# Kernel optimization log

Measured on AMD Instinct MI355X. Metric: run time of the kernel, lower is better.

The kernel has to match this reference:

```python
import jax, jax.numpy as jnp
import numpy as np

D_MODEL = 768
D_STATE = 16
D_CONV = 4
EXPAND = 2
N_LAYERS = 2
HEADDIM = 64
PATCH_DIM = 256
D_INNER = EXPAND * D_MODEL            # 1536
NHEADS = D_INNER // HEADDIM           # 24
CONV_DIM = D_INNER + 2 * D_STATE      # 1568 (x, B, C share the conv)
D_IN_PROJ = 2 * D_INNER + 2 * D_STATE + NHEADS  # 3128


def _mamba2(u, w_in, conv_w, conv_b, dt_bias, A_log, D, norm_w, w_out):
    """Mamba2 block (ngroups=1, rmsnorm=True, non-fused reference path)."""
    b, l, _ = u.shape
    zxbcdt = u @ w_in                                   # (b,l,D_IN_PROJ)
    z = zxbcdt[..., :D_INNER]
    xBC = zxbcdt[..., D_INNER:D_INNER + CONV_DIM]
    dt = jax.nn.softplus(zxbcdt[..., D_INNER + CONV_DIM:] + dt_bias)  # (b,l,H)
    # causal depthwise conv1d over L, then silu
    kernel = conv_w.T[:, None, :]                       # (D_CONV,1,CONV_DIM)
    xBC = jax.lax.conv_general_dilated(
        xBC, kernel, (1,), [(D_CONV - 1, 0)],
        dimension_numbers=('NLC', 'LIO', 'NLC'),
        feature_group_count=CONV_DIM) + conv_b
    xBC = jax.nn.silu(xBC)
    x = xBC[..., :D_INNER].reshape(b, l, NHEADS, HEADDIM)
    B = xBC[..., D_INNER:D_INNER + D_STATE]             # (b,l,N)
    C = xBC[..., D_INNER + D_STATE:]                    # (b,l,N)
    A = -jnp.exp(A_log)                                 # (H,)

    def step(h, inp):
        dt_t, x_t, b_t, c_t = inp                       # (b,H),(b,H,P),(b,N),(b,N)
        dA = jnp.exp(dt_t * A)                          # (b,H)
        h = h * dA[:, :, None, None] + jnp.einsum('bh,bhp,bn->bhpn', dt_t, x_t, b_t)
        y_t = jnp.einsum('bhpn,bn->bhp', h, c_t)
        return h, y_t

    h0 = jnp.zeros((b, NHEADS, HEADDIM, D_STATE), u.dtype)
    _, y = jax.lax.scan(step, h0,
                        (dt.swapaxes(0, 1), x.swapaxes(0, 1),
                         B.swapaxes(0, 1), C.swapaxes(0, 1)))
    y = y.swapaxes(0, 1) + x * D[:, None]               # skip: D per head
    y = y.reshape(b, l, D_INNER)
    # gated RMSNorm: rmsnorm(y * silu(z)) * weight
    g = y * jax.nn.silu(z)
    g = g * jax.lax.rsqrt(jnp.mean(g * g, axis=-1, keepdims=True) + 1e-5)
    y = g * norm_w
    return y @ w_out


def _backbone(patch_embeddings, Wp, bp, in_w, conv_w, conv_b, dt_bias,
              A_log, Dh, norm_w, out_w, bi_w, ls, fin_w):
    x = patch_embeddings @ Wp + bp
    for i in range(N_LAYERS):
        h_f = _mamba2(x, in_w[i, 0], conv_w[i, 0], conv_b[i, 0], dt_bias[i, 0],
                      A_log[i, 0], Dh[i, 0], norm_w[i, 0], out_w[i, 0])
        h_b = jnp.flip(_mamba2(jnp.flip(x, 1), in_w[i, 1], conv_w[i, 1],
                               conv_b[i, 1], dt_bias[i, 1], A_log[i, 1],
                               Dh[i, 1], norm_w[i, 1], out_w[i, 1]), 1)
        m = jnp.concatenate([h_f, h_b], axis=-1) @ bi_w[i]
        x = x + m * ls[i]
    # final RMSNorm with unit offset
    v = jnp.mean(x * x, axis=-1, keepdims=True)
    return x * jax.lax.rsqrt(v + 1e-6) * (1.0 + fin_w)


def setup_inputs() -> dict:
    key = jax.random.key(0)
    ks = jax.random.split(key, 14)
    L2 = (N_LAYERS, 2)
    pe = jax.random.normal(ks[0], (2, 2048, PATCH_DIM), jnp.float32)
    Wp = jax.random.normal(ks[1], (PATCH_DIM, D_MODEL), jnp.float32) * 0.02
    bp = jnp.zeros((D_MODEL,), jnp.float32)
    in_w = jax.random.normal(ks[2], L2 + (D_MODEL, D_IN_PROJ), jnp.float32) * 0.02
    conv_w = jax.random.normal(ks[3], L2 + (CONV_DIM, D_CONV), jnp.float32) * 0.2
    conv_b = jnp.zeros(L2 + (CONV_DIM,), jnp.float32)
    dt_bias = jax.random.uniform(ks[4], L2 + (NHEADS,), jnp.float32, -4.0, -2.0)
    A_log = jnp.log(jax.random.uniform(ks[5], L2 + (NHEADS,), jnp.float32, 1.0, 16.0))
    Dh = jax.random.normal(ks[6], L2 + (NHEADS,), jnp.float32) * 0.1 + 1.0
    norm_w = jnp.ones(L2 + (D_INNER,), jnp.float32)
    out_w = jax.random.normal(ks[7], L2 + (D_INNER, D_MODEL), jnp.float32) * 0.02
    bi_w = jax.random.normal(ks[8], (N_LAYERS, 2 * D_MODEL, D_MODEL), jnp.float32) * 0.02
    ls = jnp.full((N_LAYERS, D_MODEL), 1e-4, jnp.float32)
    fin_w = jnp.zeros((D_MODEL,), jnp.float32)
    return {"patch_embeddings": pe, "Wp": Wp, "bp": bp, "in_w": in_w,
            "conv_w": conv_w, "conv_b": conv_b, "dt_bias": dt_bias,
            "A_log": A_log, "Dh": Dh, "norm_w": norm_w, "out_w": out_w,
            "bi_w": bi_w, "ls": ls, "fin_w": fin_w}


def reference(patch_embeddings, Wp, bp, in_w, conv_w, conv_b, dt_bias,
              A_log, Dh, norm_w, out_w, bi_w, ls, fin_w):
    return _backbone(patch_embeddings, Wp, bp, in_w, conv_w, conv_b, dt_bias,
                     A_log, Dh, norm_w, out_w, bi_w, ls, fin_w)
```

## Files before the change

kernel.cpp:

```cpp
#include <hip/hip_runtime.h>

typedef unsigned short u16;
typedef short s16x8 __attribute__((ext_vector_type(8)));
typedef u16 u16x8 __attribute__((ext_vector_type(8)));
typedef float f32x4 __attribute__((ext_vector_type(4)));

__device__ inline float bf2f(u16 u) {
    union { unsigned int i; float f; } w; w.i = ((unsigned int)u) << 16; return w.f;
}
__device__ inline u16 f2bf(float f) {
    union { float f; unsigned int i; } w; w.f = f;
    unsigned int u = w.i;
    u += 0x7fffu + ((u >> 16) & 1u);
    return (u16)(u >> 16);
}

__global__ __launch_bounds__(256)
void wtransT(const float* __restrict__ src, u16* __restrict__ dst,
             int K, int N, int dstride, int src_z, int dz_hi, int dz_lo)
{
    int z = blockIdx.z;
    src += (size_t)z * src_z;
    dst += (size_t)(z >> 1) * dz_hi + (size_t)(z & 1) * dz_lo;
    __shared__ float t[32][33];
    int kt = blockIdx.y * 32, nt0 = blockIdx.x * 32;
    int lx = threadIdx.x & 31, ly = threadIdx.x >> 5;
#pragma unroll
    for (int i = 0; i < 32; i += 8) {
        int k = kt + ly + i, n = nt0 + lx;
        t[ly + i][lx] = (k < K && n < N) ? src[(size_t)k * N + n] : 0.f;
    }
    __syncthreads();
#pragma unroll
    for (int i = 0; i < 32; i += 8) {
        int n = nt0 + ly + i, k = kt + lx;
        if (n < N && k < K) dst[(size_t)n * dstride + k] = f2bf(t[lx][ly + i]);
    }
}

__global__ void cvtk(const float* __restrict__ src, u16* __restrict__ dst, int n) {
    int i = blockIdx.x * 256 + threadIdx.x;
    if (i < n) dst[i] = f2bf(src[i]);
}

__global__ __launch_bounds__(256, 2)
void gemm8(const u16* __restrict__ A, const u16* __restrict__ WT,
           int M, int N, int K,
           u16* __restrict__ bout, int ostride)
{
    __shared__ u16 lds8[2 * 16384];

    int mt, nt;
    {
        int nwg = gridDim.x * gridDim.y;
        int f = blockIdx.y * gridDim.x + blockIdx.x;
        int q = nwg >> 3, r = nwg & 7;
        int xcd = f & 7, lo = f >> 3;
        int wid = (xcd < r ? xcd * (q + 1) : r * (q + 1) + (xcd - r) * q) + lo;
        mt = wid % gridDim.y; nt = wid / gridDim.y;
    }

    const int tid  = threadIdx.x;
    const int lane = tid & 63;
    const int wave = tid >> 6;
    const int wm = wave >> 1, wn = wave & 1;
    const int r16 = lane & 15;
    const int lg  = lane >> 4;
    const int mb  = mt * 128;
    const int nb  = nt * 128;
    const int wbase = tid & 192;

    f32x4 acc[4][4];
#pragma unroll
    for (int mi = 0; mi < 4; mi++)
#pragma unroll
        for (int ni = 0; ni < 4; ni++)
            acc[mi][ni] = (f32x4){0.f, 0.f, 0.f, 0.f};

    auto stage = [&](int buf, int k0) {
        u16* bA = &lds8[buf * 16384];
        u16* bB = bA + 8192;
#pragma unroll
        for (int r = 0; r < 4; r++) {
            int e = r * 256 + tid;
            int row = e >> 3;
            int cbs = (e & 7) ^ (row & 7);
            const u16* g = A + (size_t)(mb + row) * K + k0 + cbs * 8;
            __builtin_amdgcn_global_load_lds(
                (const __attribute__((address_space(1))) void*)g,
                (__attribute__((address_space(3))) void*)&bA[(r * 256 + wbase) * 8],
                16, 0, 0);
        }
#pragma unroll
        for (int r = 0; r < 4; r++) {
            int e = r * 256 + tid;
            int row = e >> 3;
            int cbs = (e & 7) ^ (row & 7);
            const u16* g = WT + (size_t)(nb + row) * K + k0 + cbs * 8;
            __builtin_amdgcn_global_load_lds(
                (const __attribute__((address_space(1))) void*)g,
                (__attribute__((address_space(3))) void*)&bB[(r * 256 + wbase) * 8],
                16, 0, 0);
        }
    };

    const int ntk = K >> 6;
    stage(0, 0);
    stage(1, 64);
    asm volatile("s_waitcnt vmcnt(8)" ::: "memory");
    __builtin_amdgcn_sched_barrier(0);
    __builtin_amdgcn_s_barrier();

    for (int t = 0; t < ntk; t++) {
        const int buf = t & 1;
        const u16* bA = &lds8[buf * 16384];
        const u16* bB = bA + 8192;
        s16x8 a[4][2], b[4][2];
#pragma unroll
        for (int mf = 0; mf < 4; mf++)
#pragma unroll
            for (int kk = 0; kk < 2; kk++) {
                int row = wm * 64 + mf * 16 + r16;
                int cb = (kk * 4 + lg) ^ (row & 7);
                a[mf][kk] = *(const s16x8*)&bA[row * 64 + cb * 8];
            }
#pragma unroll
        for (int nf = 0; nf < 4; nf++)
#pragma unroll
            for (int kk = 0; kk < 2; kk++) {
                int row = wn * 64 + nf * 16 + r16;
                int cb = (kk * 4 + lg) ^ (row & 7);
                b[nf][kk] = *(const s16x8*)&bB[row * 64 + cb * 8];
            }
        asm volatile("s_waitcnt lgkmcnt(0)" ::: "memory");
        __builtin_amdgcn_sched_barrier(0);
        __builtin_amdgcn_s_barrier();
        if (t + 2 < ntk) {
            stage(buf, (t + 2) << 6);
            asm volatile("s_waitcnt vmcnt(8)" ::: "memory");
        } else {
            asm volatile("s_waitcnt vmcnt(0)" ::: "memory");
        }
        __builtin_amdgcn_sched_barrier(0);
        __builtin_amdgcn_s_barrier();
        __builtin_amdgcn_s_setprio(1);
#pragma unroll
        for (int mf = 0; mf < 4; mf++)
#pragma unroll
            for (int nf = 0; nf < 4; nf++) {
                acc[mf][nf] = __builtin_amdgcn_mfma_f32_16x16x32_bf16(
                    a[mf][0], b[nf][0], acc[mf][nf], 0, 0, 0);
                acc[mf][nf] = __builtin_amdgcn_mfma_f32_16x16x32_bf16(
                    a[mf][1], b[nf][1], acc[mf][nf], 0, 0, 0);
            }
        __builtin_amdgcn_s_setprio(0);
    }

#pragma unroll
    for (int mf = 0; mf < 4; mf++) {
        const int rowb = mb + wm * 64 + mf * 16 + lg * 4;
#pragma unroll
        for (int nf = 0; nf < 4; nf++) {
            int col = nb + wn * 64 + nf * 16 + r16;
            if (col < N) {
#pragma unroll
                for (int j = 0; j < 4; j++)
                    bout[(size_t)(rowb + j) * ostride + col] = f2bf(acc[mf][nf][j]);
            }
        }
    }
}

__global__ __launch_bounds__(256, 2)
void gemm9(const u16* __restrict__ A, const u16* __restrict__ WT, int K,
           float* __restrict__ fout, u16* __restrict__ bout,
           const float* __restrict__ lsv)
{
    __shared__ u16 lds9[2 * 12288];

    int mt, nt;
    {
        int nwg = gridDim.x * gridDim.y;
        int f = blockIdx.y * gridDim.x + blockIdx.x;
        int q = nwg >> 3, r = nwg & 7;
        int xcd = f & 7, lo = f >> 3;
        int wid = (xcd < r ? xcd * (q + 1) : r * (q + 1) + (xcd - r) * q) + lo;
        mt = wid % gridDim.y; nt = wid / gridDim.y;
    }

    const int tid  = threadIdx.x;
    const int lane = tid & 63;
    const int wave = tid >> 6;
    const int wm = wave >> 1, wn = wave & 1;
    const int r16 = lane & 15;
    const int lg  = lane >> 4;
    const int mb  = mt * 128;
    const int nb  = nt * 64;
    const int wbase = tid & 192;

    f32x4 acc[4][2];
#pragma unroll
    for (int mi = 0; mi < 4; mi++)
#pragma unroll
        for (int ni = 0; ni < 2; ni++)
            acc[mi][ni] = (f32x4){0.f, 0.f, 0.f, 0.f};

    auto stage = [&](int buf, int k0) {
        u16* bA = &lds9[buf * 12288];
#pragma unroll
        for (int rr = 0; rr < 6; rr++) {
            int e = rr * 256 + tid;
            int row = e >> 3;
            int cbs = (e & 7) ^ (row & 7);
            const u16* g = (rr < 4)
                ? A  + (size_t)(mb + row) * K + k0 + cbs * 8
                : WT + (size_t)(nb + row - 128) * K + k0 + cbs * 8;
            __builtin_amdgcn_global_load_lds(
                (const __attribute__((address_space(1))) void*)g,
                (__attribute__((address_space(3))) void*)&bA[(rr * 256 + wbase) * 8],
                16, 0, 0);
        }
    };

    const int ntk = K >> 6;
    stage(0, 0);
    stage(1, 64);
    asm volatile("s_waitcnt vmcnt(6)" ::: "memory");
    __builtin_amdgcn_sched_barrier(0);
    __builtin_amdgcn_s_barrier();

    for (int t = 0; t < ntk; t++) {
        const int buf = t & 1;
        const u16* bA = &lds9[buf * 12288];
        const u16* bB = bA + 8192;
        s16x8 a[4][2], b[2][2];
#pragma unroll
        for (int mf = 0; mf < 4; mf++)
#pragma unroll
            for (int kk = 0; kk < 2; kk++) {
                int row = wm * 64 + mf * 16 + r16;
                int cb = (kk * 4 + lg) ^ (row & 7);
                a[mf][kk] = *(const s16x8*)&bA[row * 64 + cb * 8];
            }
#pragma unroll
        for (int nf = 0; nf < 2; nf++)
#pragma unroll
            for (int kk = 0; kk < 2; kk++) {
                int row = wn * 32 + nf * 16 + r16;
                int cb = (kk * 4 + lg) ^ (row & 7);
                b[nf][kk] = *(const s16x8*)&bB[row * 64 + cb * 8];
            }
        asm volatile("s_waitcnt lgkmcnt(0)" ::: "memory");
        __builtin_amdgcn_sched_barrier(0);
        __builtin_amdgcn_s_barrier();
        if (t + 2 < ntk) {
            stage(buf, (t + 2) << 6);
            asm volatile("s_waitcnt vmcnt(6)" ::: "memory");
        } else {
            asm volatile("s_waitcnt vmcnt(0)" ::: "memory");
        }
        __builtin_amdgcn_sched_barrier(0);
        __builtin_amdgcn_s_barrier();
        __builtin_amdgcn_s_setprio(1);
#pragma unroll
        for (int mf = 0; mf < 4; mf++)
#pragma unroll
            for (int nf = 0; nf < 2; nf++) {
                acc[mf][nf] = __builtin_amdgcn_mfma_f32_16x16x32_bf16(
                    a[mf][0], b[nf][0], acc[mf][nf], 0, 0, 0);
                acc[mf][nf] = __builtin_amdgcn_mfma_f32_16x16x32_bf16(
                    a[mf][1], b[nf][1], acc[mf][nf], 0, 0, 0);
            }
        __builtin_amdgcn_s_setprio(0);
    }

#pragma unroll
    for (int mf = 0; mf < 4; mf++) {
        const int rowb = mb + wm * 64 + mf * 16 + lg * 4;
#pragma unroll
        for (int nf = 0; nf < 2; nf++) {
            int col = nb + wn * 32 + nf * 16 + r16;
#pragma unroll
            for (int j = 0; j < 4; j++) {
                size_t o = (size_t)(rowb + j) * 768 + col;
                float xv = fout[o] + acc[mf][nf][j] * lsv[col];
                fout[o] = xv; bout[o] = f2bf(xv);
            }
        }
    }
}

template<int BM, int BN, int EPI>
__global__ __launch_bounds__(256)
void gemmL(const u16* __restrict__ A, const u16* __restrict__ WT,
           int M, int N, int K,
           float* __restrict__ fout, u16* __restrict__ bout,
           const float* __restrict__ bias, const float* __restrict__ lsv,
           int ostride, int ocoloff,
           size_t aZ, size_t wZ, size_t oZ, int ocolZ)
{
    constexpr int MI = BM / 32, NI = BN / 32;
    constexpr int BUF = (BM + BN) * 32;
    constexpr int RA = BM / 64, RB = BN / 64;
    __shared__ u16 lds[2 * BUF];

    {
        int z = blockIdx.z;
        A += (size_t)z * aZ; WT += (size_t)z * wZ;
        bout += (size_t)(z >> 1) * oZ; ocoloff += (z & 1) * ocolZ;
    }

    int mt, nt;
    {
        int nwg = gridDim.x * gridDim.y;
        int f = blockIdx.y * gridDim.x + blockIdx.x;
        int q = nwg >> 3, r = nwg & 7;
        int xcd = f & 7, lo = f >> 3;
        int wid = (xcd < r ? xcd * (q + 1) : r * (q + 1) + (xcd - r) * q) + lo;
        mt = wid % gridDim.y; nt = wid / gridDim.y;
    }

    const int tid  = threadIdx.x;
    const int lane = tid & 63;
    const int wave = tid >> 6;
    const int wm = wave >> 1, wn = wave & 1;
    const int r16 = lane & 15;
    const int ks  = (lane >> 4) * 8;
    const int mb  = mt * BM;
    const int nb  = nt * BN;
    const int wbase = tid & 192;

    f32x4 acc[MI][NI];
#pragma unroll
    for (int mi = 0; mi < MI; mi++)
#pragma unroll
        for (int ni = 0; ni < NI; ni++)
            acc[mi][ni] = (f32x4){0.f, 0.f, 0.f, 0.f};

    auto stage = [&](int buf, int k0) {
        u16* bufA = &lds[buf * BUF];
        u16* bufB = &lds[buf * BUF + BM * 32];
#pragma unroll
        for (int r = 0; r < RA; r++) {
            int c = r * 256 + tid;
            const u16* g = A + (size_t)(mb + (c >> 2)) * K + k0 + (c & 3) * 8;
            __builtin_amdgcn_global_load_lds(
                (const __attribute__((address_space(1))) void*)g,
                (__attribute__((address_space(3))) void*)&bufA[(r * 256 + wbase) * 8],
                16, 0, 0);
        }
#pragma unroll
        for (int r = 0; r < RB; r++) {
            int c = r * 256 + tid;
            const u16* g = WT + (size_t)(nb + (c >> 2)) * K + k0 + (c & 3) * 8;
            __builtin_amdgcn_global_load_lds(
                (const __attribute__((address_space(1))) void*)g,
                (__attribute__((address_space(3))) void*)&bufB[(r * 256 + wbase) * 8],
                16, 0, 0);
        }
    };
    auto compute = [&](int buf) {
        const u16* bufA = &lds[buf * BUF];
        const u16* bufB = &lds[buf * BUF + BM * 32];
        s16x8 af[MI], bfr[NI];
#pragma unroll
        for (int mi = 0; mi < MI; mi++)
            af[mi] = *(const s16x8*)&bufA[(wm * (BM / 2) + mi * 16 + r16) * 32 + ks];
#pragma unroll
        for (int ni = 0; ni < NI; ni++)
            bfr[ni] = *(const s16x8*)&bufB[(wn * (BN / 2) + ni * 16 + r16) * 32 + ks];
#pragma unroll
        for (int mi = 0; mi < MI; mi++)
#pragma unroll
            for (int ni = 0; ni < NI; ni++)
                acc[mi][ni] = __builtin_amdgcn_mfma_f32_16x16x32_bf16(
                    af[mi], bfr[ni], acc[mi][ni], 0, 0, 0);
    };

    const int nt2 = K >> 5;
    stage(0, 0);
    __syncthreads();
    for (int t = 0; t < nt2; t++) {
        if (t + 1 < nt2) stage((t + 1) & 1, (t + 1) << 5);
        compute(t & 1);
        __syncthreads();
    }

#pragma unroll
    for (int mi = 0; mi < MI; mi++) {
        const int rowb = mb + wm * (BM / 2) + mi * 16 + (lane >> 4) * 4;
#pragma unroll
        for (int ni = 0; ni < NI; ni++) {
            int col = nb + wn * (BN / 2) + ni * 16 + r16;
            if (col < N) {
#pragma unroll
                for (int j = 0; j < 4; j++) {
                    int row = rowb + j;
                    float v = acc[mi][ni][j];
                    if (EPI == 0) {
                        v += bias[col];
                        size_t o = (size_t)row * ostride + col;
                        fout[o] = v; bout[o] = f2bf(v);
                    } else if (EPI == 1) {
                        bout[(size_t)row * ostride + ocoloff + col] = f2bf(v);
                    } else {
                        size_t o = (size_t)row * 768 + col;
                        float xv = fout[o] + v * lsv[col];
                        fout[o] = xv; bout[o] = f2bf(xv);
                    }
                }
            }
        }
    }
}

__global__ void dtk(const u16* __restrict__ zxAll, float* __restrict__ dtAll,
                    const float* __restrict__ dtb)
{
    int idx = blockIdx.x * 256 + threadIdx.x;
    if (idx >= 2 * 4096 * 24) return;
    int dir = idx / (4096 * 24);
    int r   = idx % (4096 * 24);
    int row = r / 24, h = r % 24;
    float raw = bf2f(zxAll[(size_t)row * 6256 + dir * 3128 + 3104 + h]) + dtb[dir * 24 + h];
    dtAll[((size_t)dir * 4096 + row) * 24 + h] = raw > 20.f ? raw : log1pf(__expf(raw));
}

__global__ __launch_bounds__(256)
void scan1k(const u16* __restrict__ zxAll, const float* __restrict__ dtAll,
            const float* __restrict__ cw, const float* __restrict__ cb,
            const float* __restrict__ Alog, const float* __restrict__ Dhp,
            u16* __restrict__ yAll, float* __restrict__ states, float* __restrict__ decays)
{
    const int c   = blockIdx.x;
    const int bh  = blockIdx.y;
    const int dir = blockIdx.z;
    const int b = bh / 24, h = bh % 24;
    const float* dtp = dtAll + (size_t)dir * 4096 * 24;
    u16* yp = yAll + dir * 1536;
    const float Av = -__expf(Alog[dir * 24 + h]);
    const float Dv = Dhp[dir * 24 + h];
    const int inst = (dir * 2 + b) * 24 + h;

    const int tid  = threadIdx.x;
    const int lane = tid & 63;
    const int wave = tid >> 6;
    const int r16  = lane & 15;
    const int ks   = (lane >> 4) * 8;

    __shared__ u16 xT[64][72];
    __shared__ u16 Gs[64][72];
    __shared__ u16 Bs[64][40];
    __shared__ u16 Cs[64][40];
    __shared__ u16 SBT[16][72];
    __shared__ float dts[64], cds[64];

    const u16* zxd = zxAll + dir * 3128 + 1536;
    auto growp = [&](int ii) -> const u16* {
        int l = dir ? (2047 - ii) : ii;
        return zxd + ((size_t)b * 2048 + l) * 6256;
    };
    auto rowof = [&](int t) -> size_t {
        int i = c * 64 + t;
        int l = dir ? (2047 - i) : i;
        return (size_t)b * 2048 + l;
    };
    const u16x8 zz = {0,0,0,0,0,0,0,0};

    {
        int tr = tid >> 2, pg = tid & 3;
        int chb = h * 64 + pg * 16;
        int i0 = c * 64 + tr;
        u16x8 tv[4][2];
#pragma unroll
        for (int k = 0; k < 4; k++) {
            int ii = i0 - 3 + k;
            if (ii >= 0) {
                const u16* s = growp(ii) + chb;
                tv[k][0] = *(const u16x8*)s;
                tv[k][1] = *(const u16x8*)(s + 8);
            } else { tv[k][0] = zz; tv[k][1] = zz; }
        }
        const float* cwp = cw + ((size_t)dir * 1568 + chb) * 4;
        const float* cbp = cb + (size_t)dir * 1568 + chb;
#pragma unroll
        for (int j = 0; j < 16; j++) {
            f32x4 wj = *(const f32x4*)(cwp + j * 4);
            float a = cbp[j];
            int hi = j >> 3, lo2 = j & 7;
            a += bf2f(tv[0][hi][lo2]) * wj[0] + bf2f(tv[1][hi][lo2]) * wj[1]
               + bf2f(tv[2][hi][lo2]) * wj[2] + bf2f(tv[3][hi][lo2]) * wj[3];
            a = a / (1.f + __expf(-a));
            xT[pg * 16 + j][tr] = f2bf(a);
        }
    }
    {
        int t = tid & 63, which = tid >> 6;
        if (which < 2) {
            int chb = 1536 + which * 16;
            int i0 = c * 64 + t;
            u16x8 tv[4][2];
#pragma unroll
            for (int k = 0; k < 4; k++) {
                int ii = i0 - 3 + k;
                if (ii >= 0) {
                    const u16* s = growp(ii) + chb;
                    tv[k][0] = *(const u16x8*)s;
                    tv[k][1] = *(const u16x8*)(s + 8);
                } else { tv[k][0] = zz; tv[k][1] = zz; }
            }
            const float* cwp = cw + ((size_t)dir * 1568 + chb) * 4;
            const float* cbp = cb + (size_t)dir * 1568 + chb;
            u16* dst = which ? &Cs[t][0] : &Bs[t][0];
#pragma unroll
            for (int j = 0; j < 16; j++) {
                f32x4 wj = *(const f32x4*)(cwp + j * 4);
                float a = cbp[j];
                int hi = j >> 3, lo2 = j & 7;
                a += bf2f(tv[0][hi][lo2]) * wj[0] + bf2f(tv[1][hi][lo2]) * wj[1]
                   + bf2f(tv[2][hi][lo2]) * wj[2] + bf2f(tv[3][hi][lo2]) * wj[3];
                a = a / (1.f + __expf(-a));
                dst[j] = f2bf(a);
            }
        } else {
            u16* dst = (which == 2) ? &Bs[t][16] : &Cs[t][16];
            *(u16x8*)dst = zz; *(u16x8*)(dst + 8) = zz;
        }
    }
    if (tid < 64) {
        float v = dtp[rowof(tid) * 24 + h];
        dts[tid] = v;
        float s = v;
#pragma unroll
        for (int o = 1; o < 64; o <<= 1) {
            float nvl = __shfl_up(s, o, 64);
            if (lane >= o) s += nvl;
        }
        cds[tid] = s;
    }
    __syncthreads();

    {
        const s16x8 af = *(const s16x8*)&Cs[wave * 16 + r16][ks];
#pragma unroll
        for (int st = 0; st < 4; st++) {
            const s16x8 bfr = *(const s16x8*)&Bs[st * 16 + r16][ks];
            f32x4 a2 = {0.f, 0.f, 0.f, 0.f};
            a2 = __builtin_amdgcn_mfma_f32_16x16x32_bf16(af, bfr, a2, 0, 0, 0);
            int s = st * 16 + (lane & 15);
            int tbase = wave * 16 + (lane >> 4) * 4;
            float cs = cds[s], dtv = dts[s];
#pragma unroll
            for (int j = 0; j < 4; j++) {
                int t = tbase + j;
                float g = 0.f;
                if (s <= t) {
                    g = a2[j] * dtv * __expf(Av * (cds[t] - cs));
                    if (s == t) g += Dv;
                }
                Gs[t][s] = f2bf(g);
            }
        }
    }
    {
        float cdT = cds[63];
        int s = tid & 63;
        float sc = __expf(Av * (cdT - cds[s])) * dts[s];
#pragma unroll
        for (int it = 0; it < 4; it++) {
            int n = (tid >> 6) + it * 4;
            SBT[n][s] = f2bf(sc * bf2f(Bs[s][n]));
        }
    }
    __syncthreads();

    {
#pragma unroll
        for (int pt = 0; pt < 4; pt++) {
            f32x4 a2 = {0.f, 0.f, 0.f, 0.f};
#pragma unroll
            for (int kk = 0; kk < 2; kk++) {
                s16x8 af = *(const s16x8*)&Gs[wave * 16 + r16][kk * 32 + ks];
                s16x8 bfr = *(const s16x8*)&xT[pt * 16 + r16][kk * 32 + ks];
                a2 = __builtin_amdgcn_mfma_f32_16x16x32_bf16(af, bfr, a2, 0, 0, 0);
            }
            int p = pt * 16 + (lane & 15);
            int tbase = wave * 16 + (lane >> 4) * 4;
#pragma unroll
            for (int j = 0; j < 4; j++) {
                size_t row = rowof(tbase + j);
                yp[row * 3072 + h * 64 + p] = f2bf(a2[j]);
            }
        }
    }
    {
        f32x4 a2 = {0.f, 0.f, 0.f, 0.f};
#pragma unroll
        for (int kk = 0; kk < 2; kk++) {
            s16x8 af = *(const s16x8*)&xT[wave * 16 + r16][kk * 32 + ks];
            s16x8 bfr = *(const s16x8*)&SBT[r16][kk * 32 + ks];
            a2 = __builtin_amdgcn_mfma_f32_16x16x32_bf16(af, bfr, a2, 0, 0, 0);
        }
        int n = lane & 15;
        int pbase = wave * 16 + (lane >> 4) * 4;
        float* st = states + ((size_t)inst * 32 + c) * 1024;
#pragma unroll
        for (int j = 0; j < 4; j++) st[(pbase + j) * 16 + n] = a2[j];
        if (tid == 0) decays[inst * 32 + c] = __expf(Av * cds[63]);
    }
}

__global__ __launch_bounds__(256)
void scan2k(float* __restrict__ states, const float* __restrict__ decays)
{
    int inst = blockIdx.x;
    int tid = threadIdx.x;
    float* base = states + (size_t)inst * 32 * 1024 + tid * 4;
    const float* dec = decays + inst * 32;
    f32x4 hreg = {0.f, 0.f, 0.f, 0.f};
    f32x4 L = *(f32x4*)base;
    for (int cc = 0; cc < 32; cc++) {
        f32x4 Lnext;
        if (cc + 1 < 32) Lnext = *(f32x4*)(base + (cc + 1) * 1024);
        *(f32x4*)(base + cc * 1024) = hreg;
        float d = dec[cc];
        hreg = hreg * d + L;
        L = Lnext;
    }
}

__global__ __launch_bounds__(256)
void scan3k(const float* __restrict__ states,
            const u16* __restrict__ zxAll, const float* __restrict__ dtAll,
            const float* __restrict__ cw, const float* __restrict__ cb,
            const float* __restrict__ Alog, u16* __restrict__ yAll)
{
    const int c   = blockIdx.x + 1;
    const int bh  = blockIdx.y;
    const int dir = blockIdx.z;
    const int b = bh / 24, h = bh % 24;
    const float* dtp = dtAll + (size_t)dir * 4096 * 24;
    u16* yp = yAll + dir * 1536;
    const float Av = -__expf(Alog[dir * 24 + h]);
    const int inst = (dir * 2 + b) * 24 + h;
    const int tid = threadIdx.x;

    __shared__ float hs[64][20];
    __shared__ u16 Cs3[64][16];
    __shared__ float ets[64];

    const u16* zxd = zxAll + dir * 3128 + 1536;
    auto growp = [&](int ii) -> const u16* {
        int l = dir ? (2047 - ii) : ii;
        return zxd + ((size_t)b * 2048 + l) * 6256;
    };
    auto rowof = [&](int t) -> size_t {
        int i = c * 64 + t;
        int l = dir ? (2047 - i) : i;
        return (size_t)b * 2048 + l;
    };

    {
        const float* sp = states + ((size_t)inst * 32 + c) * 1024 + tid * 4;
        f32x4 v = *(const f32x4*)sp;
        int e = tid * 4;
        int p = e >> 4, n = e & 15;
        hs[p][n] = v[0]; hs[p][n+1] = v[1]; hs[p][n+2] = v[2]; hs[p][n+3] = v[3];
    }
    if (tid < 64) {
        int i0 = c * 64 + tid;
        u16x8 tv[4][2];
#pragma unroll
        for (int k = 0; k < 4; k++) {
            const u16* s = growp(i0 - 3 + k) + 1552;
            tv[k][0] = *(const u16x8*)s;
            tv[k][1] = *(const u16x8*)(s + 8);
        }
        const float* cwp = cw + ((size_t)dir * 1568 + 1552) * 4;
        const float* cbp = cb + (size_t)dir * 1568 + 1552;
#pragma unroll
        for (int j = 0; j < 16; j++) {
            f32x4 wj = *(const f32x4*)(cwp + j * 4);
            float a = cbp[j];
            int hi = j >> 3, lo2 = j & 7;
            a += bf2f(tv[0][hi][lo2]) * wj[0] + bf2f(tv[1][hi][lo2]) * wj[1]
               + bf2f(tv[2][hi][lo2]) * wj[2] + bf2f(tv[3][hi][lo2]) * wj[3];
            a = a / (1.f + __expf(-a));
            Cs3[tid][j] = f2bf(a);
        }
        float v = dtp[rowof(tid) * 24 + h];
        float s = v;
#pragma unroll
        for (int o = 1; o < 64; o <<= 1) {
            float nvl = __shfl_up(s, o, 64);
            if ((tid & 63) >= o) s += nvl;
        }
        ets[tid] = __expf(Av * s);
    }
    __syncthreads();

    int t = tid >> 2, pg = tid & 3;
    float cv[16];
    float et = ets[t];
#pragma unroll
    for (int n = 0; n < 16; n++) cv[n] = bf2f(Cs3[t][n]) * et;
    size_t row = rowof(t);
    u16* yrow = yp + row * 3072 + h * 64 + pg * 16;
    u16x8 ya = *(u16x8*)yrow;
    u16x8 yb = *(u16x8*)(yrow + 8);
#pragma unroll
    for (int jj = 0; jj < 16; jj++) {
        int p = pg * 16 + jj;
        float acc = 0.f;
#pragma unroll
        for (int q = 0; q < 4; q++) {
            f32x4 hv = *(const f32x4*)&hs[p][q * 4];
            acc += cv[q*4]*hv[0] + cv[q*4+1]*hv[1] + cv[q*4+2]*hv[2] + cv[q*4+3]*hv[3];
        }
        if (jj < 8) ya[jj] = f2bf(bf2f(ya[jj]) + acc);
        else        yb[jj - 8] = f2bf(bf2f(yb[jj - 8]) + acc);
    }
    *(u16x8*)yrow = ya;
    *(u16x8*)(yrow + 8) = yb;
}

__global__ __launch_bounds__(256)
void gatek(const u16* __restrict__ zxAll, u16* __restrict__ yAll,
           const float* __restrict__ nw)
{
    int row = blockIdx.x, dir = blockIdx.y;
    const u16* zx = zxAll + (size_t)row * 6256 + dir * 3128;
    u16* y = yAll + (size_t)row * 3072 + dir * 1536;
    const float* nwp = nw + dir * 1536;
    int tid = threadIdx.x;
    float g[6]; float s = 0.f;
#pragma unroll
    for (int j = 0; j < 6; j++) {
        int c = j * 256 + tid;
        float z  = bf2f(zx[c]);
        float yv = bf2f(y[c]);
        float gv = yv * z / (1.f + __expf(-z));
        g[j] = gv; s += gv * gv;
    }
    __shared__ float red[4];
    for (int o = 32; o; o >>= 1) s += __shfl_down(s, o, 64);
    if ((tid & 63) == 0) red[tid >> 6] = s;
    __syncthreads();
    s = red[0] + red[1] + red[2] + red[3];
    float sc = rsqrtf(s * (1.f / 1536.f) + 1e-5f);
#pragma unroll
    for (int j = 0; j < 6; j++) {
        int c = j * 256 + tid;
        y[c] = f2bf(g[j] * sc * nwp[c]);
    }
}

__global__ __launch_bounds__(256)
void finalk(const float* __restrict__ x, const float* __restrict__ fw, float* __restrict__ out)
{
    int row = blockIdx.x; int tid = threadIdx.x;
    const float* xr = x + (size_t)row * 768;
    float v[3]; float s = 0.f;
#pragma unroll
    for (int j = 0; j < 3; j++) {
        int c = j * 256 + tid;
        v[j] = xr[c]; s += v[j] * v[j];
    }
    __shared__ float red[4];
    for (int o = 32; o; o >>= 1) s += __shfl_down(s, o, 64);
    if ((tid & 63) == 0) red[tid >> 6] = s;
    __syncthreads();
    s = red[0] + red[1] + red[2] + red[3];
    float sc = rsqrtf(s * (1.f / 768.f) + 1e-6f);
#pragma unroll
    for (int j = 0; j < 3; j++) {
        int c = j * 256 + tid;
        out[(size_t)row * 768 + c] = v[j] * sc * (1.f + fw[c]);
    }
}

extern "C" void kernel_launch(void* const* d_in, const int* in_sizes, int n_in,
                              void* d_out, int out_size, void* d_ws, size_t ws_size,
                              hipStream_t stream)
{
    const float* pe      = (const float*)d_in[0];
    const float* Wp      = (const float*)d_in[1];
    const float* bp      = (const float*)d_in[2];
    const float* in_w    = (const float*)d_in[3];
    const float* conv_w  = (const float*)d_in[4];
    const float* conv_b  = (const float*)d_in[5];
    const float* dt_bias = (const float*)d_in[6];
    const float* A_log   = (const float*)d_in[7];
    const float* Dh      = (const float*)d_in[8];
    const float* norm_w  = (const float*)d_in[9];
    const float* out_w   = (const float*)d_in[10];
    const float* bi_w    = (const float*)d_in[11];
    const float* ls      = (const float*)d_in[12];
    const float* fin_w   = (const float*)d_in[13];

    char* wp = (char*)d_ws;
    auto alloc = [&](size_t bytes) {
        char* r = wp; wp += (bytes + 255) & ~(size_t)255; return r;
    };
    u16*   WpT    = (u16*)  alloc((size_t)768 * 256 * 2);
    u16*   inWT   = (u16*)  alloc((size_t)2 * 6272 * 768 * 2);
    u16*   outWB  = (u16*)  alloc((size_t)4 * 1536 * 768 * 2);
    u16*   biWT   = (u16*)  alloc((size_t)4 * 768 * 768 * 2);
    u16*   WcombT = (u16*)  alloc((size_t)2 * 768 * 3072 * 2);
    u16*   peB    = (u16*)  alloc((size_t)4096 * 256 * 2);
    float* x      = (float*)alloc((size_t)4096 * 768 * 4);
    u16*   xb     = (u16*)  alloc((size_t)4096 * 768 * 2);
    u16*   zxAll  = (u16*)  alloc((size_t)4096 * 6256 * 2);
    float* dtAll  = (float*)alloc((size_t)2 * 4096 * 24 * 4);
    u16*   yAll   = (u16*)  alloc((size_t)4096 * 3072 * 2);
    float* states = (float*)alloc((size_t)96 * 32 * 1024 * 4);
    float* decays = (float*)alloc((size_t)96 * 32 * 4);

    wtransT<<<dim3(24, 8, 1), 256, 0, stream>>>(Wp, WpT, 256, 768, 256, 0, 0, 0);
    wtransT<<<dim3(98, 24, 4), 256, 0, stream>>>(in_w, inWT, 768, 3128, 768,
                                                 2402304, 4816896, 2402304);
    wtransT<<<dim3(24, 24, 4), 256, 0, stream>>>(bi_w, biWT, 768, 768, 768,
                                                 589824, 1179648, 589824);
    cvtk<<<(4 * 1536 * 768 + 255) / 256, 256, 0, stream>>>(out_w, outWB, 4 * 1536 * 768);
    cvtk<<<4096, 256, 0, stream>>>(pe, peB, 4096 * 256);

    gemmL<64, 64, 1><<<dim3(24, 12, 4), 256, 0, stream>>>(
        biWT, outWB, 768, 1536, 768, nullptr, WcombT,
        nullptr, nullptr, 3072, 0,
        (size_t)589824, (size_t)1179648, (size_t)768 * 3072, 1536);

    gemmL<64, 64, 0><<<dim3(12, 64, 1), 256, 0, stream>>>(
        peB, WpT, 4096, 768, 256, x, xb, bp, nullptr, 768, 0, 0, 0, 0, 0);

    for (int i = 0; i < 2; i++) {
        gemm8<<<dim3(49, 32, 1), 256, 0, stream>>>(
            xb, inWT + (size_t)i * 6272 * 768, 4096, 6256, 768, zxAll, 6256);
        dtk<<<(2 * 4096 * 24 + 255) / 256, 256, 0, stream>>>(zxAll, dtAll, dt_bias + i * 48);
        scan1k<<<dim3(32, 48, 2), 256, 0, stream>>>(zxAll, dtAll,
                                                    conv_w + (size_t)i * 2 * 1568 * 4,
                                                    conv_b + (size_t)i * 2 * 1568,
                                                    A_log + i * 48, Dh + i * 48,
                                                    yAll, states, decays);
        scan2k<<<96, 256, 0, stream>>>(states, decays);
        scan3k<<<dim3(31, 48, 2), 256, 0, stream>>>(states, zxAll, dtAll,
                                                    conv_w + (size_t)i * 2 * 1568 * 4,
                                                    conv_b + (size_t)i * 2 * 1568,
                                                    A_log + i * 48, yAll);
        gatek<<<dim3(4096, 2), 256, 0, stream>>>(zxAll, yAll, norm_w + (size_t)i * 2 * 1536);
        gemm9<<<dim3(12, 32, 1), 256, 0, stream>>>(
            yAll, WcombT + (size_t)i * 768 * 3072, 3072, x, xb, ls + i * 768);
    }

    finalk<<<4096, 256, 0, stream>>>(x, fin_w, (float*)d_out);
}
```

Baseline: 498.3 us.

## Precompute B/C conv once in preK and specialise small GEMMs with swizzled LDS

```diff
diff --git a/kernel.cpp b/kernel.cpp
--- a/kernel.cpp
+++ b/kernel.cpp
@@ -290,26 +290,18 @@
     }
 }
 
-template<int BM, int BN, int EPI>
-__global__ __launch_bounds__(256)
-void gemmL(const u16* __restrict__ A, const u16* __restrict__ WT,
-           int M, int N, int K,
-           float* __restrict__ fout, u16* __restrict__ bout,
-           const float* __restrict__ bias, const float* __restrict__ lsv,
-           int ostride, int ocoloff,
-           size_t aZ, size_t wZ, size_t oZ, int ocolZ)
-{
-    constexpr int MI = BM / 32, NI = BN / 32;
-    constexpr int BUF = (BM + BN) * 32;
-    constexpr int RA = BM / 64, RB = BN / 64;
-    __shared__ u16 lds[2 * BUF];
+__global__ __launch_bounds__(256, 2)
+void gemm10(const u16* __restrict__ A, const u16* __restrict__ WT, int K,
+            u16* __restrict__ bout, int ostride,
+            size_t aZ, size_t wZ, size_t oZ, int ocolZ)
+{
+    __shared__ u16 ldsA[2 * 12288];
 
     {
         int z = blockIdx.z;
         A += (size_t)z * aZ; WT += (size_t)z * wZ;
-        bout += (size_t)(z >> 1) * oZ; ocoloff += (z & 1) * ocolZ;
-    }
-
+        bout += (size_t)(z >> 1) * oZ + (size_t)(z & 1) * ocolZ;
+    }
     int mt, nt;
     {
         int nwg = gridDim.x * gridDim.y;
@@ -325,109 +317,254 @@
     const int wave = tid >> 6;
     const int wm = wave >> 1, wn = wave & 1;
     const int r16 = lane & 15;
-    const int ks  = (lane >> 4) * 8;
-    const int mb  = mt * BM;
-    const int nb  = nt * BN;
+    const int lg  = lane >> 4;
+    const int mb  = mt * 128;
+    const int nb  = nt * 64;
     const int wbase = tid & 192;
 
-    f32x4 acc[MI][NI];
-#pragma unroll
-    for (int mi = 0; mi < MI; mi++)
-#pragma unroll
-        for (int ni = 0; ni < NI; ni++)
+    f32x4 acc[4][2];
+#pragma unroll
+    for (int mi = 0; mi < 4; mi++)
+#pragma unroll
+        for (int ni = 0; ni < 2; ni++)
             acc[mi][ni] = (f32x4){0.f, 0.f, 0.f, 0.f};
 
     auto stage = [&](int buf, int k0) {
-        u16* bufA = &lds[buf * BUF];
-        u16* bufB = &lds[buf * BUF + BM * 32];
-#pragma unroll
-        for (int r = 0; r < RA; r++) {
-            int c = r * 256 + tid;
-            const u16* g = A + (size_t)(mb + (c >> 2)) * K + k0 + (c & 3) * 8;
+        u16* bA = &ldsA[buf * 12288];
+#pragma unroll
+        for (int rr = 0; rr < 6; rr++) {
+            int e = rr * 256 + tid;
+            int row = e >> 3;
+            int cbs = (e & 7) ^ (row & 7);
+            const u16* g = (rr < 4)
+                ? A  + (size_t)(mb + row) * K + k0 + cbs * 8
+                : WT + (size_t)(nb + row - 128) * K + k0 + cbs * 8;
             __builtin_amdgcn_global_load_lds(
                 (const __attribute__((address_space(1))) void*)g,
-                (__attribute__((address_space(3))) void*)&bufA[(r * 256 + wbase) * 8],
+                (__attribute__((address_space(3))) void*)&bA[(rr * 256 + wbase) * 8],
                 16, 0, 0);
         }
-#pragma unroll
-        for (int r = 0; r < RB; r++) {
-            int c = r * 256 + tid;
-            const u16* g = WT + (size_t)(nb + (c >> 2)) * K + k0 + (c & 3) * 8;
+    };
+
+    const int ntk = K >> 6;
+    stage(0, 0);
+    stage(1, 64);
+    asm volatile("s_waitcnt vmcnt(6)" ::: "memory");
+    __builtin_amdgcn_sched_barrier(0);
+    __builtin_amdgcn_s_barrier();
+
+    for (int t = 0; t < ntk; t++) {
+        const int buf = t & 1;
+        const u16* bA = &ldsA[buf * 12288];
+        const u16* bB = bA + 8192;
+        s16x8 a[4][2], b[2][2];
+#pragma unroll
+        for (int mf = 0; mf < 4; mf++)
+#pragma unroll
+            for (int kk = 0; kk < 2; kk++) {
+                int row = wm * 64 + mf * 16 + r16;
+                int cb = (kk * 4 + lg) ^ (row & 7);
+                a[mf][kk] = *(const s16x8*)&bA[row * 64 + cb * 8];
+            }
+#pragma unroll
+        for (int nf = 0; nf < 2; nf++)
+#pragma unroll
+            for (int kk = 0; kk < 2; kk++) {
+                int row = wn * 32 + nf * 16 + r16;
+                int cb = (kk * 4 + lg) ^ (row & 7);
+                b[nf][kk] = *(const s16x8*)&bB[row * 64 + cb * 8];
+            }
+        asm volatile("s_waitcnt lgkmcnt(0)" ::: "memory");
+        __builtin_amdgcn_sched_barrier(0);
+        __builtin_amdgcn_s_barrier();
+        if (t + 2 < ntk) {
+            stage(buf, (t + 2) << 6);
+            asm volatile("s_waitcnt vmcnt(6)" ::: "memory");
+        } else {
+            asm volatile("s_waitcnt vmcnt(0)" ::: "memory");
+        }
+        __builtin_amdgcn_sched_barrier(0);
+        __builtin_amdgcn_s_barrier();
+        __builtin_amdgcn_s_setprio(1);
+#pragma unroll
+        for (int mf = 0; mf < 4; mf++)
+#pragma unroll
+            for (int nf = 0; nf < 2; nf++) {
+                acc[mf][nf] = __builtin_amdgcn_mfma_f32_16x16x32_bf16(
+                    a[mf][0], b[nf][0], acc[mf][nf], 0, 0, 0);
+                acc[mf][nf] = __builtin_amdgcn_mfma_f32_16x16x32_bf16(
+                    a[mf][1], b[nf][1], acc[mf][nf], 0, 0, 0);
+            }
+        __builtin_amdgcn_s_setprio(0);
+    }
+
+#pragma unroll
+    for (int mf = 0; mf < 4; mf++) {
+        const int rowb = mb + wm * 64 + mf * 16 + lg * 4;
+#pragma unroll
+        for (int nf = 0; nf < 2; nf++) {
+            int col = nb + wn * 32 + nf * 16 + r16;
+#pragma unroll
+            for (int j = 0; j < 4; j++)
+                bout[(size_t)(rowb + j) * ostride + col] = f2bf(acc[mf][nf][j]);
+        }
+    }
+}
+
+__global__ __launch_bounds__(256, 2)
+void gemm11(const u16* __restrict__ A, const u16* __restrict__ WT, int K,
+            float* __restrict__ fout, u16* __restrict__ bout,
+            const float* __restrict__ bias)
+{
+    __shared__ u16 ldsB[2 * 12288];
+
+    int mt, nt;
+    {
+        int nwg = gridDim.x * gridDim.y;
+        int f = blockIdx.y * gridDim.x + blockIdx.x;
+        int q = nwg >> 3, r = nwg & 7;
+        int xcd = f & 7, lo = f >> 3;
+        int wid = (xcd < r ? xcd * (q + 1) : r * (q + 1) + (xcd - r) * q) + lo;
+        mt = wid % gridDim.y; nt = wid / gridDim.y;
+    }
+
+    const int tid  = threadIdx.x;
+    const int lane = tid & 63;
+    const int wave = tid >> 6;
+    const int wm = wave >> 1, wn = wave & 1;
+    const int r16 = lane & 15;
+    const int lg  = lane >> 4;
+    const int mb  = mt * 128;
+    const int nb  = nt * 64;
+    const int wbase = tid & 192;
+
+    f32x4 acc[4][2];
+#pragma unroll
+    for (int mi = 0; mi < 4; mi++)
+#pragma unroll
+        for (int ni = 0; ni < 2; ni++)
+            acc[mi][ni] = (f32x4){0.f, 0.f, 0.f, 0.f};
+
+    auto stage = [&](int buf, int k0) {
+        u16* bA = &ldsB[buf * 12288];
+#pragma unroll
+        for (int rr = 0; rr < 6; rr++) {
+            int e = rr * 256 + tid;
+            int row = e >> 3;
+            int cbs = (e & 7) ^ (row & 7);
+            const u16* g = (rr < 4)
+                ? A  + (size_t)(mb + row) * K + k0 + cbs * 8
+                : WT + (size_t)(nb + row - 128) * K + k0 + cbs * 8;
             __builtin_amdgcn_global_load_lds(
                 (const __attribute__((address_space(1))) void*)g,
-                (__attribute__((address_space(3))) void*)&bufB[(r * 256 + wbase) * 8],
+                (__attribute__((address_space(3))) void*)&bA[(rr * 256 + wbase) * 8],
                 16, 0, 0);
         }
     };
-    auto compute = [&](int buf) {
-        const u16* bufA = &lds[buf * BUF];
-        const u16* bufB = &lds[buf * BUF + BM * 32];
-        s16x8 af[MI], bfr[NI];
-#pragma unroll
-        for (int mi = 0; mi < MI; mi++)
-            af[mi] = *(const s16x8*)&bufA[(wm * (BM / 2) + mi * 16 + r16) * 32 + ks];
-#pragma unroll
-        for (int ni = 0; ni < NI; ni++)
-            bfr[ni] = *(const s16x8*)&bufB[(wn * (BN / 2) + ni * 16 + r16) * 32 + ks];
-#pragma unroll
-        for (int mi = 0; mi < MI; mi++)
-#pragma unroll
-            for (int ni = 0; ni < NI; ni++)
-                acc[mi][ni] = __builtin_amdgcn_mfma_f32_16x16x32_bf16(
-                    af[mi], bfr[ni], acc[mi][ni], 0, 0, 0);
-    };
-
-    const int nt2 = K >> 5;
+
+    const int ntk = K >> 6;
     stage(0, 0);
-    __syncthreads();
-    for (int t = 0; t < nt2; t++) {
-        if (t + 1 < nt2) stage((t + 1) & 1, (t + 1) << 5);
-        compute(t & 1);
-        __syncthreads();
-    }
-
-#pragma unroll
-    for (int mi = 0; mi < MI; mi++) {
-        const int rowb = mb + wm * (BM / 2) + mi * 16 + (lane >> 4) * 4;
-#pragma unroll
-        for (int ni = 0; ni < NI; ni++) {
-            int col = nb + wn * (BN / 2) + ni * 16 + r16;
-            if (col < N) {
-#pragma unroll
-                for (int j = 0; j < 4; j++) {
-                    int row = rowb + j;
-                    float v = acc[mi][ni][j];
-                    if (EPI == 0) {
-                        v += bias[col];
-                        size_t o = (size_t)row * ostride + col;
-                        fout[o] = v; bout[o] = f2bf(v);
-                    } else if (EPI == 1) {
-                        bout[(size_t)row * ostride + ocoloff + col] = f2bf(v);
-                    } else {
-                        size_t o = (size_t)row * 768 + col;
-                        float xv = fout[o] + v * lsv[col];
-                        fout[o] = xv; bout[o] = f2bf(xv);
-                    }
-                }
-            }
-        }
-    }
-}
-
-__global__ void dtk(const u16* __restrict__ zxAll, float* __restrict__ dtAll,
-                    const float* __restrict__ dtb)
+    stage(1, 64);
+    asm volatile("s_waitcnt vmcnt(6)" ::: "memory");
+    __builtin_amdgcn_sched_barrier(0);
+    __builtin_amdgcn_s_barrier();
+
+    for (int t = 0; t < ntk; t++) {
+        const int buf = t & 1;
+        const u16* bA = &ldsB[buf * 12288];
+        const u16* bB = bA + 8192;
+        s16x8 a[4][2], b[2][2];
+#pragma unroll
+        for (int mf = 0; mf < 4; mf++)
+#pragma unroll
+            for (int kk = 0; kk < 2; kk++) {
+                int row = wm * 64 + mf * 16 + r16;
+                int cb = (kk * 4 + lg) ^ (row & 7);
+                a[mf][kk] = *(const s16x8*)&bA[row * 64 + cb * 8];
+            }
+#pragma unroll
+        for (int nf = 0; nf < 2; nf++)
+#pragma unroll
+            for (int kk = 0; kk < 2; kk++) {
+                int row = wn * 32 + nf * 16 + r16;
+                int cb = (kk * 4 + lg) ^ (row & 7);
+                b[nf][kk] = *(const s16x8*)&bB[row * 64 + cb * 8];
+            }
+        asm volatile("s_waitcnt lgkmcnt(0)" ::: "memory");
+        __builtin_amdgcn_sched_barrier(0);
+        __builtin_amdgcn_s_barrier();
+        if (t + 2 < ntk) {
+            stage(buf, (t + 2) << 6);
+            asm volatile("s_waitcnt vmcnt(6)" ::: "memory");
+        } else {
+            asm volatile("s_waitcnt vmcnt(0)" ::: "memory");
+        }
+        __builtin_amdgcn_sched_barrier(0);
+        __builtin_amdgcn_s_barrier();
+        __builtin_amdgcn_s_setprio(1);
+#pragma unroll
+        for (int mf = 0; mf < 4; mf++)
+#pragma unroll
+            for (int nf = 0; nf < 2; nf++) {
+                acc[mf][nf] = __builtin_amdgcn_mfma_f32_16x16x32_bf16(
+                    a[mf][0], b[nf][0], acc[mf][nf], 0, 0, 0);
+                acc[mf][nf] = __builtin_amdgcn_mfma_f32_16x16x32_bf16(
+                    a[mf][1], b[nf][1], acc[mf][nf], 0, 0, 0);
+            }
+        __builtin_amdgcn_s_setprio(0);
+    }
+
+#pragma unroll
+    for (int mf = 0; mf < 4; mf++) {
+        const int rowb = mb + wm * 64 + mf * 16 + lg * 4;
+#pragma unroll
+        for (int nf = 0; nf < 2; nf++) {
+            int col = nb + wn * 32 + nf * 16 + r16;
+#pragma unroll
+            for (int j = 0; j < 4; j++) {
+                float v = acc[mf][nf][j] + bias[col];
+                size_t o = (size_t)(rowb + j) * 768 + col;
+                fout[o] = v; bout[o] = f2bf(v);
+            }
+        }
+    }
+}
+
+__global__ void preK(const u16* __restrict__ zxAll, float* __restrict__ dtAll,
+                     u16* __restrict__ bcAll, const float* __restrict__ dtb,
+                     const float* __restrict__ cw, const float* __restrict__ cb)
 {
     int idx = blockIdx.x * 256 + threadIdx.x;
-    if (idx >= 2 * 4096 * 24) return;
-    int dir = idx / (4096 * 24);
-    int r   = idx % (4096 * 24);
-    int row = r / 24, h = r % 24;
-    float raw = bf2f(zxAll[(size_t)row * 6256 + dir * 3128 + 3104 + h]) + dtb[dir * 24 + h];
-    dtAll[((size_t)dir * 4096 + row) * 24 + h] = raw > 20.f ? raw : log1pf(__expf(raw));
+    if (idx < 2 * 4096 * 24) {
+        int dir = idx / (4096 * 24);
+        int r   = idx % (4096 * 24);
+        int row = r / 24, h = r % 24;
+        float raw = bf2f(zxAll[(size_t)row * 6256 + dir * 3128 + 3104 + h]) + dtb[dir * 24 + h];
+        dtAll[((size_t)dir * 4096 + row) * 24 + h] = raw > 20.f ? raw : log1pf(__expf(raw));
+        return;
+    }
+    int v = idx - 2 * 4096 * 24;
+    if (v >= 2 * 4096 * 32) return;
+    int ch  = v & 31;
+    int row = (v >> 5) & 4095;
+    int dir = v >> 17;
+    int l   = row & 2047;
+    int chg = 1536 + ch;
+    float acc = cb[dir * 1568 + chg];
+    const float* w = cw + ((size_t)dir * 1568 + chg) * 4;
+#pragma unroll
+    for (int k = 0; k < 4; k++) {
+        int ll = dir ? (l + 3 - k) : (l - 3 + k);
+        if (ll >= 0 && ll < 2048)
+            acc += bf2f(zxAll[(size_t)(row + (ll - l)) * 6256 + dir * 3128 + chg]) * w[k];
+    }
+    acc = acc / (1.f + __expf(-acc));
+    bcAll[((size_t)dir * 4096 + row) * 32 + ch] = f2bf(acc);
 }
 
 __global__ __launch_bounds__(256)
 void scan1k(const u16* __restrict__ zxAll, const float* __restrict__ dtAll,
+            const u16* __restrict__ bcAll,
             const float* __restrict__ cw, const float* __restrict__ cb,
             const float* __restrict__ Alog, const float* __restrict__ Dhp,
             u16* __restrict__ yAll, float* __restrict__ states, float* __restrict__ decays)
@@ -437,6 +574,7 @@
     const int dir = blockIdx.z;
     const int b = bh / 24, h = bh % 24;
     const float* dtp = dtAll + (size_t)dir * 4096 * 24;
+    const u16* bcp = bcAll + (size_t)dir * 4096 * 32;
     u16* yp = yAll + dir * 1536;
     const float Av = -__expf(Alog[dir * 24 + h]);
     const float Dv = Dhp[dir * 24 + h];
@@ -497,31 +635,10 @@
     {
         int t = tid & 63, which = tid >> 6;
         if (which < 2) {
-            int chb = 1536 + which * 16;
-            int i0 = c * 64 + t;
-            u16x8 tv[4][2];
-#pragma unroll
-            for (int k = 0; k < 4; k++) {
-                int ii = i0 - 3 + k;
-                if (ii >= 0) {
-                    const u16* s = growp(ii) + chb;
-                    tv[k][0] = *(const u16x8*)s;
-                    tv[k][1] = *(const u16x8*)(s + 8);
-                } else { tv[k][0] = zz; tv[k][1] = zz; }
-            }
-            const float* cwp = cw + ((size_t)dir * 1568 + chb) * 4;
-            const float* cbp = cb + (size_t)dir * 1568 + chb;
+            const u16* src = bcp + rowof(t) * 32 + which * 16;
             u16* dst = which ? &Cs[t][0] : &Bs[t][0];
-#pragma unroll
-            for (int j = 0; j < 16; j++) {
-                f32x4 wj = *(const f32x4*)(cwp + j * 4);
-                float a = cbp[j];
-                int hi = j >> 3, lo2 = j & 7;
-                a += bf2f(tv[0][hi][lo2]) * wj[0] + bf2f(tv[1][hi][lo2]) * wj[1]
-                   + bf2f(tv[2][hi][lo2]) * wj[2] + bf2f(tv[3][hi][lo2]) * wj[3];
-                a = a / (1.f + __expf(-a));
-                dst[j] = f2bf(a);
-            }
+            *(u16x8*)dst = *(const u16x8*)src;
+            *(u16x8*)(dst + 8) = *(const u16x8*)(src + 8);
         } else {
             u16* dst = (which == 2) ? &Bs[t][16] : &Cs[t][16];
             *(u16x8*)dst = zz; *(u16x8*)(dst + 8) = zz;
@@ -631,8 +748,7 @@
 
 __global__ __launch_bounds__(256)
 void scan3k(const float* __restrict__ states,
-            const u16* __restrict__ zxAll, const float* __restrict__ dtAll,
-            const float* __restrict__ cw, const float* __restrict__ cb,
+            const u16* __restrict__ bcAll, const float* __restrict__ dtAll,
             const float* __restrict__ Alog, u16* __restrict__ yAll)
 {
     const int c   = blockIdx.x + 1;
@@ -640,6 +756,7 @@
     const int dir = blockIdx.z;
     const int b = bh / 24, h = bh % 24;
     const float* dtp = dtAll + (size_t)dir * 4096 * 24;
+    const u16* bcp = bcAll + (size_t)dir * 4096 * 32;
     u16* yp = yAll + dir * 1536;
     const float Av = -__expf(Alog[dir * 24 + h]);
     const int inst = (dir * 2 + b) * 24 + h;
@@ -649,11 +766,6 @@
     __shared__ u16 Cs3[64][16];
     __shared__ float ets[64];
 
-    const u16* zxd = zxAll + dir * 3128 + 1536;
-    auto growp = [&](int ii) -> const u16* {
-        int l = dir ? (2047 - ii) : ii;
-        return zxd + ((size_t)b * 2048 + l) * 6256;
-    };
     auto rowof = [&](int t) -> size_t {
         int i = c * 64 + t;
         int l = dir ? (2047 - i) : i;
@@ -668,27 +780,11 @@
         hs[p][n] = v[0]; hs[p][n+1] = v[1]; hs[p][n+2] = v[2]; hs[p][n+3] = v[3];
     }
     if (tid < 64) {
-        int i0 = c * 64 + tid;
-        u16x8 tv[4][2];
-#pragma unroll
-        for (int k = 0; k < 4; k++) {
-            const u16* s = growp(i0 - 3 + k) + 1552;
-            tv[k][0] = *(const u16x8*)s;
-            tv[k][1] = *(const u16x8*)(s + 8);
-        }
-        const float* cwp = cw + ((size_t)dir * 1568 + 1552) * 4;
-        const float* cbp = cb + (size_t)dir * 1568 + 1552;
-#pragma unroll
-        for (int j = 0; j < 16; j++) {
-            f32x4 wj = *(const f32x4*)(cwp + j * 4);
-            float a = cbp[j];
-            int hi = j >> 3, lo2 = j & 7;
-            a += bf2f(tv[0][hi][lo2]) * wj[0] + bf2f(tv[1][hi][lo2]) * wj[1]
-               + bf2f(tv[2][hi][lo2]) * wj[2] + bf2f(tv[3][hi][lo2]) * wj[3];
-            a = a / (1.f + __expf(-a));
-            Cs3[tid][j] = f2bf(a);
-        }
-        float v = dtp[rowof(tid) * 24 + h];
+        size_t row = rowof(tid);
+        const u16* src = bcp + row * 32 + 16;
+        *(u16x8*)&Cs3[tid][0] = *(const u16x8*)src;
+        *(u16x8*)&Cs3[tid][8] = *(const u16x8*)(src + 8);
+        float v = dtp[row * 24 + h];
         float s = v;
 #pragma unroll
         for (int o = 1; o < 64; o <<= 1) {
@@ -812,6 +908,7 @@
     u16*   xb     = (u16*)  alloc((size_t)4096 * 768 * 2);
     u16*   zxAll  = (u16*)  alloc((size_t)4096 * 6256 * 2);
     float* dtAll  = (float*)alloc((size_t)2 * 4096 * 24 * 4);
+    u16*   bcAll  = (u16*)  alloc((size_t)2 * 4096 * 32 * 2);
     u16*   yAll   = (u16*)  alloc((size_t)4096 * 3072 * 2);
     float* states = (float*)alloc((size_t)96 * 32 * 1024 * 4);
     float* decays = (float*)alloc((size_t)96 * 32 * 4);
@@ -824,27 +921,25 @@
     cvtk<<<(4 * 1536 * 768 + 255) / 256, 256, 0, stream>>>(out_w, outWB, 4 * 1536 * 768);
     cvtk<<<4096, 256, 0, stream>>>(pe, peB, 4096 * 256);
 
-    gemmL<64, 64, 1><<<dim3(24, 12, 4), 256, 0, stream>>>(
-        biWT, outWB, 768, 1536, 768, nullptr, WcombT,
-        nullptr, nullptr, 3072, 0,
+    gemm10<<<dim3(24, 6, 4), 256, 0, stream>>>(
+        biWT, outWB, 768, WcombT, 3072,
         (size_t)589824, (size_t)1179648, (size_t)768 * 3072, 1536);
 
-    gemmL<64, 64, 0><<<dim3(12, 64, 1), 256, 0, stream>>>(
-        peB, WpT, 4096, 768, 256, x, xb, bp, nullptr, 768, 0, 0, 0, 0, 0);
+    gemm11<<<dim3(12, 32), 256, 0, stream>>>(peB, WpT, 256, x, xb, bp);
 
     for (int i = 0; i < 2; i++) {
         gemm8<<<dim3(49, 32, 1), 256, 0, stream>>>(
             xb, inWT + (size_t)i * 6272 * 768, 4096, 6256, 768, zxAll, 6256);
-        dtk<<<(2 * 4096 * 24 + 255) / 256, 256, 0, stream>>>(zxAll, dtAll, dt_bias + i * 48);
-        scan1k<<<dim3(32, 48, 2), 256, 0, stream>>>(zxAll, dtAll,
+        preK<<<(2 * 4096 * 56 + 255) / 256, 256, 0, stream>>>(
+            zxAll, dtAll, bcAll, dt_bias + i * 48,
+            conv_w + (size_t)i * 2 * 1568 * 4, conv_b + (size_t)i * 2 * 1568);
+        scan1k<<<dim3(32, 48, 2), 256, 0, stream>>>(zxAll, dtAll, bcAll,
                                                     conv_w + (size_t)i * 2 * 1568 * 4,
                                                     conv_b + (size_t)i * 2 * 1568,
                                                     A_log + i * 48, Dh + i * 48,
                                                     yAll, states, decays);
         scan2k<<<96, 256, 0, stream>>>(states, decays);
-        scan3k<<<dim3(31, 48, 2), 256, 0, stream>>>(states, zxAll, dtAll,
-                                                    conv_w + (size_t)i * 2 * 1568 * 4,
-                                                    conv_b + (size_t)i * 2 * 1568,
+        scan3k<<<dim3(31, 48, 2), 256, 0, stream>>>(states, bcAll, dtAll,
                                                     A_log + i * 48, yAll);
         gatek<<<dim3(4096, 2), 256, 0, stream>>>(zxAll, yAll, norm_w + (size_t)i * 2 * 1536);
         gemm9<<<dim3(12, 32, 1), 256, 0, stream>>>(
```

Result: faster. 475.2 us (-4.6%).
